# Optimization experiments

Hardware: AMD Instinct MI355X
Metric: run time of the kernel (lower is better)

The kernel has to match this reference:

```python
import jax, jax.numpy as jnp
import numpy as np

WS = 8         # window size (square)
SHIFT = 4      # shift size
NUM_HEADS = 8

def _layernorm(x, g, b, eps=1e-5):
    m = x.mean(-1, keepdims=True)
    v = ((x - m) ** 2).mean(-1, keepdims=True)
    return (x - m) / jnp.sqrt(v + eps) * g + b

def _rel_index():
    # relative_position_index for num_frames_q = num_frames_kv = 1 (d-term is 0)
    ch = np.arange(WS)
    coords = np.stack(np.meshgrid(ch, ch, indexing='ij'))      # (2, WS, WS)
    flat = coords.reshape(2, -1)                                 # (2, N)
    rel = flat[:, :, None] - flat[:, None, :]                    # (2, N, N)
    idx = (rel[0] + WS - 1) * (2 * WS - 1) + (rel[1] + WS - 1)   # (N, N)
    return jnp.asarray(idx, dtype=jnp.int32)

def setup_inputs() -> dict:
    key = jax.random.key(0)
    ks = jax.random.split(key, 16)
    B, D, H, W, C = 2, 2, 256, 256, 256
    hid = 4 * C
    nW = (H // WS) * (W // WS)
    N = WS * WS
    f = jax.random.normal
    return {
        'x': f(ks[0], (B, D, H, W, C), jnp.float32),
        'mask_matrix': f(ks[1], (nW, N, N), jnp.float32),
        'g1': jnp.ones((C,), jnp.float32),
        'b1': jnp.zeros((C,), jnp.float32),
        'qw': f(ks[2], (C, C), jnp.float32) * 0.02,
        'qb': jnp.zeros((C,), jnp.float32),
        'kvw': f(ks[3], (2 * C, C), jnp.float32) * 0.02,
        'kvb': jnp.zeros((2 * C,), jnp.float32),
        'pw': f(ks[4], (C, C), jnp.float32) * 0.02,
        'pb': jnp.zeros((C,), jnp.float32),
        'bias_table': f(ks[5], ((2 * WS - 1) ** 2, NUM_HEADS), jnp.float32) * 0.02,
        'g2': jnp.ones((C,), jnp.float32),
        'b2': jnp.zeros((C,), jnp.float32),
        'w1': f(ks[6], (hid, C), jnp.float32) * 0.02,
        'bi1': jnp.zeros((hid,), jnp.float32),
        'w2': f(ks[7], (C, hid), jnp.float32) * 0.02,
        'bi2': jnp.zeros((C,), jnp.float32),
    }

def reference(x, mask_matrix, g1, b1, qw, qb, kvw, kvb, pw, pb, bias_table, g2, b2, w1, bi1, w2, bi2):
    B, D, H, W, C = x.shape
    h = NUM_HEADS
    d = C // h
    N = WS * WS
    nH, nWc = H // WS, W // WS
    nwin = nH * nWc

    shortcut = x[:, 0]                       # (B, H, W, C)  (frame 0)
    xn = _layernorm(x, g1, b1)
    xs = jnp.roll(xn, (-SHIFT, -SHIFT), axis=(2, 3))   # cyclic shift

    # window partition: (B, D, H, W, C) -> (B*nwin, D, N, C)
    win = xs.reshape(B, D, nH, WS, nWc, WS, C)
    win = win.transpose(0, 2, 4, 1, 3, 5, 6).reshape(B * nwin, D, N, C)
    q_in = win[:, 0]                          # (B_, N, C) query = frame 0
    kv_in = win[:, 1]                         # (B_, N, C) kv    = frame 1

    q = (q_in @ qw.T + qb).reshape(-1, N, h, d).transpose(0, 2, 1, 3) * (d ** -0.5)
    kv = (kv_in @ kvw.T + kvb).reshape(-1, N, 2, h, d).transpose(2, 0, 3, 1, 4)
    k, v = kv[0], kv[1]                       # (B_, h, N, d)

    attn = jnp.einsum('bhnd,bhmd->bhnm', q, k)            # (B_, h, N, N)
    bias = bias_table[_rel_index()]                        # (N, N, h)
    attn = attn + bias.transpose(2, 0, 1)[None]
    attn = attn.reshape(B, nwin, h, N, N) + mask_matrix[None, :, None]
    attn = jax.nn.softmax(attn.reshape(-1, h, N, N), axis=-1)

    out = jnp.einsum('bhnm,bhmd->bhnd', attn, v)          # (B_, h, N, d)
    out = out.transpose(0, 2, 1, 3).reshape(-1, N, C)
    out = out @ pw.T + pb + q_in                           # residual inside attn

    # window reverse: (B*nwin, N, C) -> (B, H, W, C)
    out = out.reshape(B, nH, nWc, WS, WS, C).transpose(0, 1, 3, 2, 4, 5).reshape(B, H, W, C)
    out = jnp.roll(out, (SHIFT, SHIFT), axis=(1, 2))

    x1 = shortcut + out
    y = _layernorm(x1, g2, b2)
    y = jax.nn.gelu(y @ w1.T + bi1, approximate=False) @ w2.T + bi2
    return x1 + y
```

## Files before the change

kernel.cpp:

```cpp
#include <hip/hip_runtime.h>
#include <hip/hip_bf16.h>
#include <math.h>

#define SHIFT_ 4

typedef __attribute__((ext_vector_type(8))) short bh8;
typedef __attribute__((ext_vector_type(4))) short sh4;
typedef __attribute__((ext_vector_type(4))) float f4;
typedef __attribute__((ext_vector_type(8))) __bf16 bf8t;

static __device__ __forceinline__ f4 mfma16(bh8 a, bh8 b, f4 c){
  return __builtin_amdgcn_mfma_f32_16x16x32_bf16(
    __builtin_bit_cast(bf8t, a), __builtin_bit_cast(bf8t, b), c, 0, 0, 0);
}
static __device__ __forceinline__ unsigned short f2b(float f){
  unsigned u = __builtin_bit_cast(unsigned, f);
  u += 0x7fffu + ((u >> 16) & 1u);
  return (unsigned short)(u >> 16);
}
static __device__ __forceinline__ float b2f(unsigned short h){
  return __builtin_bit_cast(float, ((unsigned)h) << 16);
}
static __device__ __forceinline__ unsigned cvt_pk_bf16(float lo, float hi){
  unsigned r;
  asm("v_cvt_pk_bf16_f32 %0, %1, %2" : "=v"(r) : "v"(lo), "v"(hi));
  return r;
}
static __device__ __forceinline__ float gelu_f(float hv){
  float u = hv * (1.5957691216f + 0.0713548162f * hv * hv);
  return hv * __builtin_amdgcn_rcpf(1.f + __expf(-u));
}

__global__ __launch_bounds__(256) void prep_w(
    const float* __restrict__ qw, const float* __restrict__ kvw,
    const float* __restrict__ pw, const float* __restrict__ w1,
    const float* __restrict__ w2, unsigned short* __restrict__ wb){
  int i = blockIdx.x * 256 + threadIdx.x;
  float v;
  if      (i < 65536)  v = qw[i] * 0.17677669529663687f;
  else if (i < 196608) v = kvw[i - 65536];
  else if (i < 262144) v = pw[i - 196608];
  else if (i < 524288) v = w1[i - 262144];
  else                 v = w2[i - 524288];
  wb[i] = f2b(v);
}

__global__ __launch_bounds__(256) void ln1_win(
    const float* __restrict__ x, const float* __restrict__ g1,
    const float* __restrict__ b1,
    unsigned short* __restrict__ q_in, unsigned short* __restrict__ kv_in){
  int rid  = blockIdx.x * 4 + (threadIdx.x >> 6);
  int lane = threadIdx.x & 63;
  int d    = rid >> 17;
  int rem  = rid & 131071;
  int w = rem >> 6, n = rem & 63;
  int b = w >> 10, hb = (w >> 5) & 31, wbk = w & 31;
  int sh = (hb * 8 + (n >> 3) + SHIFT_) & 255;
  int sw = (wbk * 8 + (n & 7) + SHIFT_) & 255;
  const float* src = x + ((((size_t)(b * 2 + d)) * 256 + sh) * 256 + sw) * 256;
  float4 v = *(const float4*)(src + lane * 4);
  float s  = v.x + v.y + v.z + v.w;
  float ss = v.x * v.x + v.y * v.y + v.z * v.z + v.w * v.w;
  #pragma unroll
  for (int off = 1; off < 64; off <<= 1){ s += __shfl_xor(s, off); ss += __shfl_xor(ss, off); }
  float m    = s * (1.f / 256.f);
  float rstd = rsqrtf(ss * (1.f / 256.f) - m * m + 1e-5f);
  int c = lane * 4;
  float4 g  = *(const float4*)(g1 + c);
  float4 bb = *(const float4*)(b1 + c);
  sh4 o;
  o.x = (short)f2b((v.x - m) * rstd * g.x + bb.x);
  o.y = (short)f2b((v.y - m) * rstd * g.y + bb.y);
  o.z = (short)f2b((v.z - m) * rstd * g.z + bb.z);
  o.w = (short)f2b((v.w - m) * rstd * g.w + bb.w);
  unsigned short* dst = (d == 0 ? q_in : kv_in) + (size_t)rem * 256 + c;
  *(sh4*)dst = o;
}

template<int MODE, int NT>
__global__ __launch_bounds__(512, 4) void gemm_bt(
    const unsigned short* __restrict__ A, const unsigned short* __restrict__ Wt,
    const float* __restrict__ bias, float bias_scale,
    unsigned short* __restrict__ outb, unsigned short* __restrict__ vpl,
    float* __restrict__ outf, const unsigned short* __restrict__ qin,
    const float* __restrict__ xsrc){
  __shared__ unsigned short sA[128][64];
  __shared__ unsigned short sB[256][64];
  int m0 = blockIdx.x * 128;
  int tid = threadIdx.x, lane = tid & 63, wid = tid >> 6;
  int wm = wid >> 2, wn = wid & 3;
  int llo = lane & 15, lhi = lane >> 4;
  int lr = lane >> 3, lc = (lane & 7) * 8;
  const f4 FZ = {0.f, 0.f, 0.f, 0.f};
  for (int nt = 0; nt < NT; nt++){
    f4 acc[4][4];
    for (int i = 0; i < 4; i++) for (int j = 0; j < 4; j++) acc[i][j] = FZ;
    for (int t = 0; t < 4; t++){
      int k0 = t * 64;
      #pragma unroll
      for (int c = 0; c < 2; c++){
        int rr = wid * 16 + c * 8;
        __builtin_amdgcn_global_load_lds(
          (const __attribute__((address_space(1))) unsigned int*)(A + (size_t)(m0 + rr + lr) * 256 + k0 + lc),
          (__attribute__((address_space(3))) unsigned int*)&sA[rr][0], 16, 0, 0);
      }
      #pragma unroll
      for (int c = 0; c < 4; c++){
        int rb = wid * 32 + c * 8;
        __builtin_amdgcn_global_load_lds(
          (const __attribute__((address_space(1))) unsigned int*)(Wt + (size_t)(nt * 256 + rb + lr) * 256 + k0 + lc),
          (__attribute__((address_space(3))) unsigned int*)&sB[rb][0], 16, 0, 0);
      }
      __syncthreads();
      #pragma unroll
      for (int ks = 0; ks < 2; ks++){
        bh8 a[4], b[4];
        #pragma unroll
        for (int mi = 0; mi < 4; mi++) a[mi] = *(const bh8*)&sA[wm * 64 + mi * 16 + llo][ks * 32 + lhi * 8];
        #pragma unroll
        for (int nj = 0; nj < 4; nj++) b[nj] = *(const bh8*)&sB[wn * 64 + nj * 16 + llo][ks * 32 + lhi * 8];
        #pragma unroll
        for (int mi = 0; mi < 4; mi++)
          #pragma unroll
          for (int nj = 0; nj < 4; nj++){
            if (MODE < 2) acc[mi][nj] = mfma16(b[nj], a[mi], acc[mi][nj]);
            else          acc[mi][nj] = mfma16(a[mi], b[nj], acc[mi][nj]);
          }
      }
      __syncthreads();
    }
    if (MODE < 2){
      #pragma unroll
      for (int nj = 0; nj < 4; nj++){
        int cb = wn * 64 + nj * 16 + lhi * 4;
        int col = nt * 256 + cb;
        float4 bv = *(const float4*)(bias + col);
        #pragma unroll
        for (int mi = 0; mi < 4; mi++){
          int row = m0 + wm * 64 + mi * 16 + llo;
          float f0 = acc[mi][nj][0] + bv.x * bias_scale;
          float f1 = acc[mi][nj][1] + bv.y * bias_scale;
          float f2 = acc[mi][nj][2] + bv.z * bias_scale;
          float f3 = acc[mi][nj][3] + bv.w * bias_scale;
          uint2 p;
          p.x = cvt_pk_bf16(f0, f1);
          p.y = cvt_pk_bf16(f2, f3);
          if (MODE == 0 || nt == 0) *(uint2*)(outb + (size_t)row * 256 + cb) = p;
          else                      *(uint2*)(vpl  + (size_t)row * 256 + cb) = p;
        }
      }
    } else {
      #pragma unroll
      for (int mi = 0; mi < 4; mi++)
        #pragma unroll
        for (int nj = 0; nj < 4; nj++){
          int col = wn * 64 + nj * 16 + llo;
          float bv = bias[col] * bias_scale;
          #pragma unroll
          for (int r = 0; r < 4; r++){
            int row = m0 + wm * 64 + mi * 16 + lhi * 4 + r;
            int w = row >> 6, n = row & 63;
            int b = w >> 10, hb = (w >> 5) & 31, wbk = w & 31;
            int hh = (hb * 8 + (n >> 3) + SHIFT_) & 255;
            int ww = (wbk * 8 + (n & 7) + SHIFT_) & 255;
            float res = b2f(qin[(size_t)row * 256 + col]);
            float sc  = xsrc[((((size_t)(b * 2)) * 256 + hh) * 256 + ww) * 256 + col];
            outf[(((size_t)b * 256 + hh) * 256 + ww) * 256 + col] = acc[mi][nj][r] + bv + res + sc;
          }
        }
    }
  }
}

__global__ __launch_bounds__(256, 2) void attn_k(
    const unsigned short* __restrict__ q, const unsigned short* __restrict__ k,
    const unsigned short* __restrict__ v, const float* __restrict__ mask,
    const float* __restrict__ bias_table, unsigned short* __restrict__ aout){
  __shared__ unsigned short sMask[64][72];
  __shared__ unsigned short sVT[128][72];
  __shared__ unsigned short sP[4][64][72];
  __shared__ float sBias[4][225];
  int bid = blockIdx.x;
  int w = bid >> 1, hg = bid & 1;
  int tid = threadIdx.x, lane = tid & 63, wid = tid >> 6;
  int hd = hg * 4 + wid;
  int llo = lane & 15, lhi = lane >> 4;
  const unsigned short* qp = q + (size_t)w * 64 * 256 + hd * 32;
  const unsigned short* kp = k + (size_t)w * 64 * 256 + hd * 32;
  bh8 af[4], bf[4];
  #pragma unroll
  for (int mi = 0; mi < 4; mi++) af[mi] = *(const bh8*)(qp + (size_t)(mi * 16 + llo) * 256 + lhi * 8);
  #pragma unroll
  for (int nj = 0; nj < 4; nj++) bf[nj] = *(const bh8*)(kp + (size_t)(nj * 16 + llo) * 256 + lhi * 8);
  const float* mrow = mask + (size_t)(w & 1023) * 4096;
  #pragma unroll
  for (int i = 0; i < 2; i++){
    int base = (tid + i * 256) * 8;
    float4 u0 = *(const float4*)(mrow + base);
    float4 u1 = *(const float4*)(mrow + base + 4);
    int rr = base >> 6, cc = base & 63;
    uint4 p;
    p.x = cvt_pk_bf16(u0.x, u0.y); p.y = cvt_pk_bf16(u0.z, u0.w);
    p.z = cvt_pk_bf16(u1.x, u1.y); p.w = cvt_pk_bf16(u1.z, u1.w);
    *(uint4*)&sMask[rr][cc] = p;
  }
  {
    const unsigned short* vp = v + (size_t)w * 64 * 256 + hg * 128;
    #pragma unroll
    for (int it = 0; it < 4; it++){
      int idx = tid + it * 256;
      int n = idx >> 4, dc = (idx & 15) * 8;
      bh8 vv = *(const bh8*)(vp + (size_t)n * 256 + dc);
      #pragma unroll
      for (int j = 0; j < 8; j++) sVT[dc + j][n] = (unsigned short)vv[j];
    }
  }
  for (int i = lane; i < 225; i += 64) sBias[wid][i] = bias_table[i * 8 + hd];
  const f4 FZ = {0.f, 0.f, 0.f, 0.f};
  f4 acc[4][4];
  #pragma unroll
  for (int mi = 0; mi < 4; mi++)
    #pragma unroll
    for (int nj = 0; nj < 4; nj++)
      acc[mi][nj] = mfma16(af[mi], bf[nj], FZ);
  __syncthreads();
  #pragma unroll
  for (int mi = 0; mi < 4; mi++){
    #pragma unroll
    for (int r = 0; r < 4; r++){
      int rr = mi * 16 + lhi * 4 + r;
      int yi = rr >> 3, xi = rr & 7;
      float sv[4]; float mx = -1e30f;
      #pragma unroll
      for (int nj = 0; nj < 4; nj++){
        int cc = nj * 16 + llo;
        int idx = (yi - (cc >> 3) + 7) * 15 + (xi - (cc & 7) + 7);
        sv[nj] = acc[mi][nj][r] + sBias[wid][idx] + b2f(sMask[rr][cc]);
        mx = fmaxf(mx, sv[nj]);
      }
      #pragma unroll
      for (int off = 1; off < 16; off <<= 1) mx = fmaxf(mx, __shfl_xor(mx, off));
      float sum = 0.f;
      #pragma unroll
      for (int nj = 0; nj < 4; nj++){ sv[nj] = __expf(sv[nj] - mx); sum += sv[nj]; }
      #pragma unroll
      for (int off = 1; off < 16; off <<= 1) sum += __shfl_xor(sum, off);
      float inv = __builtin_amdgcn_rcpf(sum);
      #pragma unroll
      for (int nj = 0; nj < 4; nj++) sP[wid][rr][nj * 16 + llo] = f2b(sv[nj] * inv);
    }
  }
  f4 o[4][2];
  for (int mi = 0; mi < 4; mi++) for (int dj = 0; dj < 2; dj++) o[mi][dj] = FZ;
  #pragma unroll
  for (int ks = 0; ks < 2; ks++){
    bh8 pa[4], vb[2];
    #pragma unroll
    for (int mi = 0; mi < 4; mi++) pa[mi] = *(const bh8*)&sP[wid][mi * 16 + llo][ks * 32 + lhi * 8];
    #pragma unroll
    for (int dj = 0; dj < 2; dj++) vb[dj] = *(const bh8*)&sVT[wid * 32 + dj * 16 + llo][ks * 32 + lhi * 8];
    #pragma unroll
    for (int mi = 0; mi < 4; mi++)
      #pragma unroll
      for (int dj = 0; dj < 2; dj++)
        o[mi][dj] = mfma16(pa[mi], vb[dj], o[mi][dj]);
  }
  #pragma unroll
  for (int mi = 0; mi < 4; mi++)
    for (int dj = 0; dj < 2; dj++)
      for (int r = 0; r < 4; r++){
        int rr = mi * 16 + lhi * 4 + r, dd = dj * 16 + llo;
        aout[((size_t)w * 64 + rr) * 256 + hd * 32 + dd] = f2b(o[mi][dj][r]);
      }
}

__global__ __launch_bounds__(256) void ln2_k(
    const float* __restrict__ x1, const float* __restrict__ g2,
    const float* __restrict__ b2, unsigned short* __restrict__ xn){
  int rid  = blockIdx.x * 4 + (threadIdx.x >> 6);
  int lane = threadIdx.x & 63;
  const float* xr = x1 + (size_t)rid * 256;
  float4 v = *(const float4*)(xr + lane * 4);
  float s  = v.x + v.y + v.z + v.w;
  float ss = v.x * v.x + v.y * v.y + v.z * v.z + v.w * v.w;
  #pragma unroll
  for (int off = 1; off < 64; off <<= 1){ s += __shfl_xor(s, off); ss += __shfl_xor(ss, off); }
  float m    = s * (1.f / 256.f);
  float rstd = rsqrtf(ss * (1.f / 256.f) - m * m + 1e-5f);
  int c = lane * 4;
  float4 g  = *(const float4*)(g2 + c);
  float4 bb = *(const float4*)(b2 + c);
  sh4 o;
  o.x = (short)f2b((v.x - m) * rstd * g.x + bb.x);
  o.y = (short)f2b((v.y - m) * rstd * g.y + bb.y);
  o.z = (short)f2b((v.z - m) * rstd * g.z + bb.z);
  o.w = (short)f2b((v.w - m) * rstd * g.w + bb.w);
  *(sh4*)(xn + (size_t)rid * 256 + c) = o;
}

template<int KSTEPS, int EPI, int BIASF>
__global__ __launch_bounds__(256, 3) void mlp_gemm(
    const unsigned short* __restrict__ A, int lda,
    const unsigned short* __restrict__ Bw, int ldb,
    const float* __restrict__ bias,
    unsigned short* __restrict__ outb, int ldo,
    float* __restrict__ outf){
  __shared__ unsigned short sA[128][64];
  __shared__ unsigned short sB[128][64];
  int n0 = blockIdx.x * 128, m0 = blockIdx.y * 128;
  int tid = threadIdx.x, lane = tid & 63, wid = tid >> 6;
  int wm = wid >> 1, wn = wid & 1;
  int llo = lane & 15, lhi = lane >> 4;
  int lr = lane >> 3, lc = (lane & 7) * 8;
  const f4 FZ = {0.f, 0.f, 0.f, 0.f};
  f4 acc[4][4];
  for (int i = 0; i < 4; i++) for (int j = 0; j < 4; j++) acc[i][j] = FZ;

  for (int t = 0; t < KSTEPS; t++){
    int k0 = t * 64;
    #pragma unroll
    for (int c = 0; c < 4; c++){
      int rr = wid * 32 + c * 8 + lr;
      __builtin_amdgcn_global_load_lds(
        (const __attribute__((address_space(1))) unsigned int*)(A + (size_t)(m0 + rr) * lda + k0 + lc),
        (__attribute__((address_space(3))) unsigned int*)&sA[wid * 32 + c * 8][0], 16, 0, 0);
      __builtin_amdgcn_global_load_lds(
        (const __attribute__((address_space(1))) unsigned int*)(Bw + (size_t)(n0 + rr) * ldb + k0 + lc),
        (__attribute__((address_space(3))) unsigned int*)&sB[wid * 32 + c * 8][0], 16, 0, 0);
    }
    __syncthreads();
    #pragma unroll
    for (int ks = 0; ks < 2; ks++){
      bh8 a[4], b[4];
      #pragma unroll
      for (int mi = 0; mi < 4; mi++) a[mi] = *(const bh8*)&sA[wm * 64 + mi * 16 + llo][ks * 32 + lhi * 8];
      #pragma unroll
      for (int nj = 0; nj < 4; nj++) b[nj] = *(const bh8*)&sB[wn * 64 + nj * 16 + llo][ks * 32 + lhi * 8];
      #pragma unroll
      for (int mi = 0; mi < 4; mi++)
        #pragma unroll
        for (int nj = 0; nj < 4; nj++){
          if (EPI == 0) acc[mi][nj] = mfma16(b[nj], a[mi], acc[mi][nj]);
          else          acc[mi][nj] = mfma16(a[mi], b[nj], acc[mi][nj]);
        }
    }
    __syncthreads();
  }
  if (EPI == 0){
    #pragma unroll
    for (int nj = 0; nj < 4; nj++){
      int cb = n0 + wn * 64 + nj * 16 + lhi * 4;
      float4 bv = *(const float4*)(bias + cb);
      #pragma unroll
      for (int mi = 0; mi < 4; mi++){
        int row = m0 + wm * 64 + mi * 16 + llo;
        float g0 = gelu_f(acc[mi][nj][0] + bv.x);
        float g1 = gelu_f(acc[mi][nj][1] + bv.y);
        float g2 = gelu_f(acc[mi][nj][2] + bv.z);
        float g3 = gelu_f(acc[mi][nj][3] + bv.w);
        uint2 p;
        p.x = cvt_pk_bf16(g0, g1);
        p.y = cvt_pk_bf16(g2, g3);
        *(uint2*)(outb + (size_t)row * ldo + cb) = p;
      }
    }
  } else {
    #pragma unroll
    for (int mi = 0; mi < 4; mi++)
      #pragma unroll
      for (int nj = 0; nj < 4; nj++){
        int col = n0 + wn * 64 + nj * 16 + llo;
        float bv = BIASF ? bias[col] : 0.f;
        #pragma unroll
        for (int r = 0; r < 4; r++){
          int row = m0 + wm * 64 + mi * 16 + lhi * 4 + r;
          outf[(size_t)row * 256 + col] += acc[mi][nj][r] + bv;
        }
      }
  }
}

extern "C" void kernel_launch(void* const* d_in, const int* in_sizes, int n_in,
                              void* d_out, int out_size, void* d_ws, size_t ws_size,
                              hipStream_t stream){
  const float* x          = (const float*)d_in[0];
  const float* mask       = (const float*)d_in[1];
  const float* g1         = (const float*)d_in[2];
  const float* b1         = (const float*)d_in[3];
  const float* qw         = (const float*)d_in[4];
  const float* qb         = (const float*)d_in[5];
  const float* kvw        = (const float*)d_in[6];
  const float* kvb        = (const float*)d_in[7];
  const float* pw         = (const float*)d_in[8];
  const float* pb         = (const float*)d_in[9];
  const float* bias_table = (const float*)d_in[10];
  const float* g2         = (const float*)d_in[11];
  const float* b2         = (const float*)d_in[12];
  const float* w1         = (const float*)d_in[13];
  const float* bi1        = (const float*)d_in[14];
  const float* w2         = (const float*)d_in[15];
  const float* bi2        = (const float*)d_in[16];
  float* out = (float*)d_out;
  char* ws = (char*)d_ws;
  const long long MB = 1048576LL;
  unsigned short* wb    = (unsigned short*)(ws);
  unsigned short* q_in  = (unsigned short*)(ws + (long long)(1.5 * MB));
  unsigned short* kv_in = (unsigned short*)(ws + (long long)(65.5 * MB));
  unsigned short* qbuf  = (unsigned short*)(ws + (long long)(129.5 * MB));
  unsigned short* kbuf  = (unsigned short*)(ws + (long long)(193.5 * MB));
  unsigned short* vbuf  = (unsigned short*)(ws + (long long)(257.5 * MB));
  unsigned short* aoutb = kv_in;
  unsigned short* xn    = vbuf;
  unsigned short* Hh    = q_in;

  prep_w<<<3072, 256, 0, stream>>>(qw, kvw, pw, w1, w2, wb);
  ln1_win<<<65536, 256, 0, stream>>>(x, g1, b1, q_in, kv_in);
  gemm_bt<0, 1><<<1024, 512, 0, stream>>>(q_in, wb, qb, 0.17677669529663687f,
                                          qbuf, nullptr, nullptr, nullptr, nullptr);
  gemm_bt<1, 2><<<1024, 512, 0, stream>>>(kv_in, wb + 65536, kvb, 1.0f,
                                          kbuf, vbuf, nullptr, nullptr, nullptr);
  attn_k<<<4096, 256, 0, stream>>>(qbuf, kbuf, vbuf, mask, bias_table, aoutb);
  gemm_bt<2, 1><<<1024, 512, 0, stream>>>(aoutb, wb + 196608, pb, 1.0f,
                                          nullptr, nullptr, out, q_in, x);
  ln2_k<<<32768, 256, 0, stream>>>(out, g2, b2, xn);
  const unsigned short* w1b = wb + 262144;
  const unsigned short* w2b = wb + 524288;
  for (int h = 0; h < 2; h++){
    const long long R = (long long)h * 65536;
    mlp_gemm<4, 0, 0><<<dim3(8, 512), 256, 0, stream>>>(xn + R * 256, 256, w1b, 256,
                                                        bi1, Hh, 1024, nullptr);
    mlp_gemm<16, 1, 1><<<dim3(2, 512), 256, 0, stream>>>(Hh, 1024, w2b, 1024,
                                                         bi2, nullptr, 0, out + R * 256);
  }
}
```

Measured before the change: 768.9 us.

## Double-buffer LDS tiles in GEMM kernels and shrink MLP chunk size

Both the attention projection GEMMs and the MLP GEMMs now double-buffer their shared-memory tiles, prefetching the next K-slice with async global-to-LDS loads while the MFMA work runs on the current slice. This removes one barrier per step and hides load latency. gemm_bt moves from 512-thread blocks with a 128x256 tile to 256-thread blocks that loop over 128-wide N tiles. The MLP is split into four row chunks instead of two, so the hidden buffer fits in cache better. The costs are lower occupancy from doubled LDS and a lower launch_bounds, plus more kernel launches.

```diff
diff --git a/kernel.cpp b/kernel.cpp
--- a/kernel.cpp
+++ b/kernel.cpp
@@ -29,6 +29,11 @@
 static __device__ __forceinline__ float gelu_f(float hv){
   float u = hv * (1.5957691216f + 0.0713548162f * hv * hv);
   return hv * __builtin_amdgcn_rcpf(1.f + __expf(-u));
+}
+static __device__ __forceinline__ void glds16(const unsigned short* g, unsigned short* l){
+  __builtin_amdgcn_global_load_lds(
+    (const __attribute__((address_space(1))) unsigned int*)g,
+    (__attribute__((address_space(3))) unsigned int*)l, 16, 0, 0);
 }
 
 __global__ __launch_bounds__(256) void prep_w(
@@ -78,97 +83,101 @@
 }
 
 template<int MODE, int NT>
-__global__ __launch_bounds__(512, 4) void gemm_bt(
+__global__ __launch_bounds__(256, 2) void gemm_bt(
     const unsigned short* __restrict__ A, const unsigned short* __restrict__ Wt,
     const float* __restrict__ bias, float bias_scale,
     unsigned short* __restrict__ outb, unsigned short* __restrict__ vpl,
     float* __restrict__ outf, const unsigned short* __restrict__ qin,
     const float* __restrict__ xsrc){
-  __shared__ unsigned short sA[128][64];
-  __shared__ unsigned short sB[256][64];
+  __shared__ unsigned short sA[2][128][64];
+  __shared__ unsigned short sB[2][128][64];
   int m0 = blockIdx.x * 128;
   int tid = threadIdx.x, lane = tid & 63, wid = tid >> 6;
-  int wm = wid >> 2, wn = wid & 3;
+  int wm = wid >> 1, wn = wid & 1;
   int llo = lane & 15, lhi = lane >> 4;
   int lr = lane >> 3, lc = (lane & 7) * 8;
+  const int TT = NT * 4;
+  #pragma unroll
+  for (int c = 0; c < 4; c++){
+    int rr = wid * 32 + c * 8;
+    glds16(A  + (size_t)(m0 + rr + lr) * 256 + lc, &sA[0][rr][0]);
+    glds16(Wt + (size_t)(rr + lr) * 256 + lc,      &sB[0][rr][0]);
+  }
+  __syncthreads();
   const f4 FZ = {0.f, 0.f, 0.f, 0.f};
-  for (int nt = 0; nt < NT; nt++){
-    f4 acc[4][4];
-    for (int i = 0; i < 4; i++) for (int j = 0; j < 4; j++) acc[i][j] = FZ;
-    for (int t = 0; t < 4; t++){
-      int k0 = t * 64;
-      #pragma unroll
-      for (int c = 0; c < 2; c++){
-        int rr = wid * 16 + c * 8;
-        __builtin_amdgcn_global_load_lds(
-          (const __attribute__((address_space(1))) unsigned int*)(A + (size_t)(m0 + rr + lr) * 256 + k0 + lc),
-          (__attribute__((address_space(3))) unsigned int*)&sA[rr][0], 16, 0, 0);
-      }
+  f4 acc[4][4];
+  for (int i = 0; i < 4; i++) for (int j = 0; j < 4; j++) acc[i][j] = FZ;
+  for (int tt = 0; tt < TT; ++tt){
+    int cur = tt & 1;
+    if (tt + 1 < TT){
+      int t1 = (tt + 1) & 3, n1 = (tt + 1) >> 2;
       #pragma unroll
       for (int c = 0; c < 4; c++){
-        int rb = wid * 32 + c * 8;
-        __builtin_amdgcn_global_load_lds(
-          (const __attribute__((address_space(1))) unsigned int*)(Wt + (size_t)(nt * 256 + rb + lr) * 256 + k0 + lc),
-          (__attribute__((address_space(3))) unsigned int*)&sB[rb][0], 16, 0, 0);
-      }
-      __syncthreads();
-      #pragma unroll
-      for (int ks = 0; ks < 2; ks++){
-        bh8 a[4], b[4];
+        int rr = wid * 32 + c * 8;
+        glds16(A  + (size_t)(m0 + rr + lr) * 256 + t1 * 64 + lc,       &sA[cur ^ 1][rr][0]);
+        glds16(Wt + (size_t)(n1 * 128 + rr + lr) * 256 + t1 * 64 + lc, &sB[cur ^ 1][rr][0]);
+      }
+    }
+    #pragma unroll
+    for (int ks = 0; ks < 2; ks++){
+      bh8 a[4], b[4];
+      #pragma unroll
+      for (int mi = 0; mi < 4; mi++) a[mi] = *(const bh8*)&sA[cur][wm * 64 + mi * 16 + llo][ks * 32 + lhi * 8];
+      #pragma unroll
+      for (int nj = 0; nj < 4; nj++) b[nj] = *(const bh8*)&sB[cur][wn * 64 + nj * 16 + llo][ks * 32 + lhi * 8];
+      #pragma unroll
+      for (int mi = 0; mi < 4; mi++)
         #pragma unroll
-        for (int mi = 0; mi < 4; mi++) a[mi] = *(const bh8*)&sA[wm * 64 + mi * 16 + llo][ks * 32 + lhi * 8];
+        for (int nj = 0; nj < 4; nj++){
+          if (MODE < 2) acc[mi][nj] = mfma16(b[nj], a[mi], acc[mi][nj]);
+          else          acc[mi][nj] = mfma16(a[mi], b[nj], acc[mi][nj]);
+        }
+    }
+    if ((tt & 3) == 3){
+      int nt = tt >> 2;
+      if (MODE < 2){
         #pragma unroll
-        for (int nj = 0; nj < 4; nj++) b[nj] = *(const bh8*)&sB[wn * 64 + nj * 16 + llo][ks * 32 + lhi * 8];
+        for (int nj = 0; nj < 4; nj++){
+          int cb = wn * 64 + nj * 16 + lhi * 4;
+          int col = nt * 128 + cb;
+          float4 bv = *(const float4*)(bias + col);
+          #pragma unroll
+          for (int mi = 0; mi < 4; mi++){
+            int row = m0 + wm * 64 + mi * 16 + llo;
+            float f0 = acc[mi][nj][0] + bv.x * bias_scale;
+            float f1 = acc[mi][nj][1] + bv.y * bias_scale;
+            float f2 = acc[mi][nj][2] + bv.z * bias_scale;
+            float f3 = acc[mi][nj][3] + bv.w * bias_scale;
+            uint2 p;
+            p.x = cvt_pk_bf16(f0, f1);
+            p.y = cvt_pk_bf16(f2, f3);
+            if (MODE == 0 || col < 256) *(uint2*)(outb + (size_t)row * 256 + col) = p;
+            else                        *(uint2*)(vpl  + (size_t)row * 256 + (col - 256)) = p;
+          }
+        }
+      } else {
         #pragma unroll
         for (int mi = 0; mi < 4; mi++)
           #pragma unroll
           for (int nj = 0; nj < 4; nj++){
-            if (MODE < 2) acc[mi][nj] = mfma16(b[nj], a[mi], acc[mi][nj]);
-            else          acc[mi][nj] = mfma16(a[mi], b[nj], acc[mi][nj]);
+            int col = nt * 128 + wn * 64 + nj * 16 + llo;
+            float bv = bias[col] * bias_scale;
+            #pragma unroll
+            for (int r = 0; r < 4; r++){
+              int row = m0 + wm * 64 + mi * 16 + lhi * 4 + r;
+              int w = row >> 6, n = row & 63;
+              int b = w >> 10, hb = (w >> 5) & 31, wbk = w & 31;
+              int hh = (hb * 8 + (n >> 3) + SHIFT_) & 255;
+              int ww = (wbk * 8 + (n & 7) + SHIFT_) & 255;
+              float res = b2f(qin[(size_t)row * 256 + col]);
+              float sc  = xsrc[((((size_t)(b * 2)) * 256 + hh) * 256 + ww) * 256 + col];
+              outf[(((size_t)b * 256 + hh) * 256 + ww) * 256 + col] = acc[mi][nj][r] + bv + res + sc;
+            }
           }
       }
-      __syncthreads();
-    }
-    if (MODE < 2){
-      #pragma unroll
-      for (int nj = 0; nj < 4; nj++){
-        int cb = wn * 64 + nj * 16 + lhi * 4;
-        int col = nt * 256 + cb;
-        float4 bv = *(const float4*)(bias + col);
-        #pragma unroll
-        for (int mi = 0; mi < 4; mi++){
-          int row = m0 + wm * 64 + mi * 16 + llo;
-          float f0 = acc[mi][nj][0] + bv.x * bias_scale;
-          float f1 = acc[mi][nj][1] + bv.y * bias_scale;
-          float f2 = acc[mi][nj][2] + bv.z * bias_scale;
-          float f3 = acc[mi][nj][3] + bv.w * bias_scale;
-          uint2 p;
-          p.x = cvt_pk_bf16(f0, f1);
-          p.y = cvt_pk_bf16(f2, f3);
-          if (MODE == 0 || nt == 0) *(uint2*)(outb + (size_t)row * 256 + cb) = p;
-          else                      *(uint2*)(vpl  + (size_t)row * 256 + cb) = p;
-        }
-      }
-    } else {
-      #pragma unroll
-      for (int mi = 0; mi < 4; mi++)
-        #pragma unroll
-        for (int nj = 0; nj < 4; nj++){
-          int col = wn * 64 + nj * 16 + llo;
-          float bv = bias[col] * bias_scale;
-          #pragma unroll
-          for (int r = 0; r < 4; r++){
-            int row = m0 + wm * 64 + mi * 16 + lhi * 4 + r;
-            int w = row >> 6, n = row & 63;
-            int b = w >> 10, hb = (w >> 5) & 31, wbk = w & 31;
-            int hh = (hb * 8 + (n >> 3) + SHIFT_) & 255;
-            int ww = (wbk * 8 + (n & 7) + SHIFT_) & 255;
-            float res = b2f(qin[(size_t)row * 256 + col]);
-            float sc  = xsrc[((((size_t)(b * 2)) * 256 + hh) * 256 + ww) * 256 + col];
-            outf[(((size_t)b * 256 + hh) * 256 + ww) * 256 + col] = acc[mi][nj][r] + bv + res + sc;
-          }
-        }
-    }
+      for (int i = 0; i < 4; i++) for (int j = 0; j < 4; j++) acc[i][j] = FZ;
+    }
+    __syncthreads();
   }
 }
 
@@ -299,43 +308,48 @@
 }
 
 template<int KSTEPS, int EPI, int BIASF>
-__global__ __launch_bounds__(256, 3) void mlp_gemm(
+__global__ __launch_bounds__(256, 2) void mlp_gemm(
     const unsigned short* __restrict__ A, int lda,
     const unsigned short* __restrict__ Bw, int ldb,
     const float* __restrict__ bias,
     unsigned short* __restrict__ outb, int ldo,
     float* __restrict__ outf){
-  __shared__ unsigned short sA[128][64];
-  __shared__ unsigned short sB[128][64];
+  __shared__ unsigned short sA[2][128][64];
+  __shared__ unsigned short sB[2][128][64];
   int n0 = blockIdx.x * 128, m0 = blockIdx.y * 128;
   int tid = threadIdx.x, lane = tid & 63, wid = tid >> 6;
   int wm = wid >> 1, wn = wid & 1;
   int llo = lane & 15, lhi = lane >> 4;
   int lr = lane >> 3, lc = (lane & 7) * 8;
+  #pragma unroll
+  for (int c = 0; c < 4; c++){
+    int rr = wid * 32 + c * 8;
+    glds16(A  + (size_t)(m0 + rr + lr) * lda + lc, &sA[0][rr][0]);
+    glds16(Bw + (size_t)(n0 + rr + lr) * ldb + lc, &sB[0][rr][0]);
+  }
+  __syncthreads();
   const f4 FZ = {0.f, 0.f, 0.f, 0.f};
   f4 acc[4][4];
   for (int i = 0; i < 4; i++) for (int j = 0; j < 4; j++) acc[i][j] = FZ;
 
   for (int t = 0; t < KSTEPS; t++){
-    int k0 = t * 64;
-    #pragma unroll
-    for (int c = 0; c < 4; c++){
-      int rr = wid * 32 + c * 8 + lr;
-      __builtin_amdgcn_global_load_lds(
-        (const __attribute__((address_space(1))) unsigned int*)(A + (size_t)(m0 + rr) * lda + k0 + lc),
-        (__attribute__((address_space(3))) unsigned int*)&sA[wid * 32 + c * 8][0], 16, 0, 0);
-      __builtin_amdgcn_global_load_lds(
-        (const __attribute__((address_space(1))) unsigned int*)(Bw + (size_t)(n0 + rr) * ldb + k0 + lc),
-        (__attribute__((address_space(3))) unsigned int*)&sB[wid * 32 + c * 8][0], 16, 0, 0);
-    }
-    __syncthreads();
+    int cur = t & 1;
+    if (t + 1 < KSTEPS){
+      int k1 = (t + 1) * 64;
+      #pragma unroll
+      for (int c = 0; c < 4; c++){
+        int rr = wid * 32 + c * 8;
+        glds16(A  + (size_t)(m0 + rr + lr) * lda + k1 + lc, &sA[cur ^ 1][rr][0]);
+        glds16(Bw + (size_t)(n0 + rr + lr) * ldb + k1 + lc, &sB[cur ^ 1][rr][0]);
+      }
+    }
     #pragma unroll
     for (int ks = 0; ks < 2; ks++){
       bh8 a[4], b[4];
       #pragma unroll
-      for (int mi = 0; mi < 4; mi++) a[mi] = *(const bh8*)&sA[wm * 64 + mi * 16 + llo][ks * 32 + lhi * 8];
-      #pragma unroll
-      for (int nj = 0; nj < 4; nj++) b[nj] = *(const bh8*)&sB[wn * 64 + nj * 16 + llo][ks * 32 + lhi * 8];
+      for (int mi = 0; mi < 4; mi++) a[mi] = *(const bh8*)&sA[cur][wm * 64 + mi * 16 + llo][ks * 32 + lhi * 8];
+      #pragma unroll
+      for (int nj = 0; nj < 4; nj++) b[nj] = *(const bh8*)&sB[cur][wn * 64 + nj * 16 + llo][ks * 32 + lhi * 8];
       #pragma unroll
       for (int mi = 0; mi < 4; mi++)
         #pragma unroll
@@ -415,21 +429,21 @@
 
   prep_w<<<3072, 256, 0, stream>>>(qw, kvw, pw, w1, w2, wb);
   ln1_win<<<65536, 256, 0, stream>>>(x, g1, b1, q_in, kv_in);
-  gemm_bt<0, 1><<<1024, 512, 0, stream>>>(q_in, wb, qb, 0.17677669529663687f,
+  gemm_bt<0, 2><<<1024, 256, 0, stream>>>(q_in, wb, qb, 0.17677669529663687f,
                                           qbuf, nullptr, nullptr, nullptr, nullptr);
-  gemm_bt<1, 2><<<1024, 512, 0, stream>>>(kv_in, wb + 65536, kvb, 1.0f,
+  gemm_bt<1, 4><<<1024, 256, 0, stream>>>(kv_in, wb + 65536, kvb, 1.0f,
                                           kbuf, vbuf, nullptr, nullptr, nullptr);
   attn_k<<<4096, 256, 0, stream>>>(qbuf, kbuf, vbuf, mask, bias_table, aoutb);
-  gemm_bt<2, 1><<<1024, 512, 0, stream>>>(aoutb, wb + 196608, pb, 1.0f,
+  gemm_bt<2, 2><<<1024, 256, 0, stream>>>(aoutb, wb + 196608, pb, 1.0f,
                                           nullptr, nullptr, out, q_in, x);
   ln2_k<<<32768, 256, 0, stream>>>(out, g2, b2, xn);
   const unsigned short* w1b = wb + 262144;
   const unsigned short* w2b = wb + 524288;
-  for (int h = 0; h < 2; h++){
-    const long long R = (long long)h * 65536;
-    mlp_gemm<4, 0, 0><<<dim3(8, 512), 256, 0, stream>>>(xn + R * 256, 256, w1b, 256,
+  for (int h = 0; h < 4; h++){
+    const long long R = (long long)h * 32768;
+    mlp_gemm<4, 0, 0><<<dim3(8, 256), 256, 0, stream>>>(xn + R * 256, 256, w1b, 256,
                                                         bi1, Hh, 1024, nullptr);
-    mlp_gemm<16, 1, 1><<<dim3(2, 512), 256, 0, stream>>>(Hh, 1024, w2b, 1024,
+    mlp_gemm<16, 1, 1><<<dim3(2, 256), 256, 0, stream>>>(Hh, 1024, w2b, 1024,
                                                          bi2, nullptr, 0, out + R * 256);
   }
 }
```

Result: slower. 834.3 us (+8.5%).

## Fuse Q and KV projections into one kernel and LayerNorm2 into proj GEMM

Applied to the files above, without the earlier changes.

Merges the separate Q and KV projection GEMM launches into a single kernel that loops over the three output slices. It also folds the second LayerNorm into the output-projection GEMM epilogue, computing row statistics through shuffles and LDS and writing both the fp32 residual and the bf16 normalized activations. This removes one launch and the full re-read of the fp32 x1 tensor by the standalone ln2 kernel. In exchange the epilogue does extra LDS reductions and syncs, and it still writes with scattered per-lane stores.

```diff
diff --git a/kernel.cpp b/kernel.cpp
--- a/kernel.cpp
+++ b/kernel.cpp
@@ -29,6 +29,11 @@
 static __device__ __forceinline__ float gelu_f(float hv){
   float u = hv * (1.5957691216f + 0.0713548162f * hv * hv);
   return hv * __builtin_amdgcn_rcpf(1.f + __expf(-u));
+}
+static __device__ __forceinline__ void glds16(const unsigned short* g, unsigned short* l){
+  __builtin_amdgcn_global_load_lds(
+    (const __attribute__((address_space(1))) unsigned int*)g,
+    (__attribute__((address_space(3))) unsigned int*)l, 16, 0, 0);
 }
 
 __global__ __launch_bounds__(256) void prep_w(
@@ -77,13 +82,12 @@
   *(sh4*)dst = o;
 }
 
-template<int MODE, int NT>
-__global__ __launch_bounds__(512, 4) void gemm_bt(
-    const unsigned short* __restrict__ A, const unsigned short* __restrict__ Wt,
-    const float* __restrict__ bias, float bias_scale,
-    unsigned short* __restrict__ outb, unsigned short* __restrict__ vpl,
-    float* __restrict__ outf, const unsigned short* __restrict__ qin,
-    const float* __restrict__ xsrc){
+__global__ __launch_bounds__(512, 4) void qkv_gemm(
+    const unsigned short* __restrict__ q_in, const unsigned short* __restrict__ kv_in,
+    const unsigned short* __restrict__ wpack,
+    const float* __restrict__ qbias, const float* __restrict__ kvbias,
+    unsigned short* __restrict__ qo, unsigned short* __restrict__ ko,
+    unsigned short* __restrict__ vo){
   __shared__ unsigned short sA[128][64];
   __shared__ unsigned short sB[256][64];
   int m0 = blockIdx.x * 128;
@@ -92,7 +96,12 @@
   int llo = lane & 15, lhi = lane >> 4;
   int lr = lane >> 3, lc = (lane & 7) * 8;
   const f4 FZ = {0.f, 0.f, 0.f, 0.f};
-  for (int nt = 0; nt < NT; nt++){
+  for (int nt = 0; nt < 3; nt++){
+    const unsigned short* A  = (nt == 0) ? q_in : kv_in;
+    const unsigned short* Wt = wpack + nt * 65536;
+    const float* bias = (nt == 0) ? qbias : kvbias + (nt - 1) * 256;
+    unsigned short* outb = (nt == 0) ? qo : (nt == 1 ? ko : vo);
+    float bscale = (nt == 0) ? 0.17677669529663687f : 1.f;
     f4 acc[4][4];
     for (int i = 0; i < 4; i++) for (int j = 0; j < 4; j++) acc[i][j] = FZ;
     for (int t = 0; t < 4; t++){
@@ -100,16 +109,12 @@
       #pragma unroll
       for (int c = 0; c < 2; c++){
         int rr = wid * 16 + c * 8;
-        __builtin_amdgcn_global_load_lds(
-          (const __attribute__((address_space(1))) unsigned int*)(A + (size_t)(m0 + rr + lr) * 256 + k0 + lc),
-          (__attribute__((address_space(3))) unsigned int*)&sA[rr][0], 16, 0, 0);
+        glds16(A + (size_t)(m0 + rr + lr) * 256 + k0 + lc, &sA[rr][0]);
       }
       #pragma unroll
       for (int c = 0; c < 4; c++){
         int rb = wid * 32 + c * 8;
-        __builtin_amdgcn_global_load_lds(
-          (const __attribute__((address_space(1))) unsigned int*)(Wt + (size_t)(nt * 256 + rb + lr) * 256 + k0 + lc),
-          (__attribute__((address_space(3))) unsigned int*)&sB[rb][0], 16, 0, 0);
+        glds16(Wt + (size_t)(rb + lr) * 256 + k0 + lc, &sB[rb][0]);
       }
       __syncthreads();
       #pragma unroll
@@ -122,52 +127,27 @@
         #pragma unroll
         for (int mi = 0; mi < 4; mi++)
           #pragma unroll
-          for (int nj = 0; nj < 4; nj++){
-            if (MODE < 2) acc[mi][nj] = mfma16(b[nj], a[mi], acc[mi][nj]);
-            else          acc[mi][nj] = mfma16(a[mi], b[nj], acc[mi][nj]);
-          }
+          for (int nj = 0; nj < 4; nj++)
+            acc[mi][nj] = mfma16(b[nj], a[mi], acc[mi][nj]);
       }
       __syncthreads();
     }
-    if (MODE < 2){
-      #pragma unroll
-      for (int nj = 0; nj < 4; nj++){
-        int cb = wn * 64 + nj * 16 + lhi * 4;
-        int col = nt * 256 + cb;
-        float4 bv = *(const float4*)(bias + col);
-        #pragma unroll
-        for (int mi = 0; mi < 4; mi++){
-          int row = m0 + wm * 64 + mi * 16 + llo;
-          float f0 = acc[mi][nj][0] + bv.x * bias_scale;
-          float f1 = acc[mi][nj][1] + bv.y * bias_scale;
-          float f2 = acc[mi][nj][2] + bv.z * bias_scale;
-          float f3 = acc[mi][nj][3] + bv.w * bias_scale;
-          uint2 p;
-          p.x = cvt_pk_bf16(f0, f1);
-          p.y = cvt_pk_bf16(f2, f3);
-          if (MODE == 0 || nt == 0) *(uint2*)(outb + (size_t)row * 256 + cb) = p;
-          else                      *(uint2*)(vpl  + (size_t)row * 256 + cb) = p;
-        }
-      }
-    } else {
-      #pragma unroll
-      for (int mi = 0; mi < 4; mi++)
-        #pragma unroll
-        for (int nj = 0; nj < 4; nj++){
-          int col = wn * 64 + nj * 16 + llo;
-          float bv = bias[col] * bias_scale;
-          #pragma unroll
-          for (int r = 0; r < 4; r++){
-            int row = m0 + wm * 64 + mi * 16 + lhi * 4 + r;
-            int w = row >> 6, n = row & 63;
-            int b = w >> 10, hb = (w >> 5) & 31, wbk = w & 31;
-            int hh = (hb * 8 + (n >> 3) + SHIFT_) & 255;
-            int ww = (wbk * 8 + (n & 7) + SHIFT_) & 255;
-            float res = b2f(qin[(size_t)row * 256 + col]);
-            float sc  = xsrc[((((size_t)(b * 2)) * 256 + hh) * 256 + ww) * 256 + col];
-            outf[(((size_t)b * 256 + hh) * 256 + ww) * 256 + col] = acc[mi][nj][r] + bv + res + sc;
-          }
-        }
+    #pragma unroll
+    for (int nj = 0; nj < 4; nj++){
+      int cb = wn * 64 + nj * 16 + lhi * 4;
+      float4 bv = *(const float4*)(bias + cb);
+      #pragma unroll
+      for (int mi = 0; mi < 4; mi++){
+        int row = m0 + wm * 64 + mi * 16 + llo;
+        float f0 = acc[mi][nj][0] + bv.x * bscale;
+        float f1 = acc[mi][nj][1] + bv.y * bscale;
+        float f2 = acc[mi][nj][2] + bv.z * bscale;
+        float f3 = acc[mi][nj][3] + bv.w * bscale;
+        uint2 p;
+        p.x = cvt_pk_bf16(f0, f1);
+        p.y = cvt_pk_bf16(f2, f3);
+        *(uint2*)(outb + (size_t)row * 256 + cb) = p;
+      }
     }
   }
 }
@@ -274,28 +254,123 @@
       }
 }
 
-__global__ __launch_bounds__(256) void ln2_k(
-    const float* __restrict__ x1, const float* __restrict__ g2,
-    const float* __restrict__ b2, unsigned short* __restrict__ xn){
-  int rid  = blockIdx.x * 4 + (threadIdx.x >> 6);
-  int lane = threadIdx.x & 63;
-  const float* xr = x1 + (size_t)rid * 256;
-  float4 v = *(const float4*)(xr + lane * 4);
-  float s  = v.x + v.y + v.z + v.w;
-  float ss = v.x * v.x + v.y * v.y + v.z * v.z + v.w * v.w;
-  #pragma unroll
-  for (int off = 1; off < 64; off <<= 1){ s += __shfl_xor(s, off); ss += __shfl_xor(ss, off); }
-  float m    = s * (1.f / 256.f);
-  float rstd = rsqrtf(ss * (1.f / 256.f) - m * m + 1e-5f);
-  int c = lane * 4;
-  float4 g  = *(const float4*)(g2 + c);
-  float4 bb = *(const float4*)(b2 + c);
-  sh4 o;
-  o.x = (short)f2b((v.x - m) * rstd * g.x + bb.x);
-  o.y = (short)f2b((v.y - m) * rstd * g.y + bb.y);
-  o.z = (short)f2b((v.z - m) * rstd * g.z + bb.z);
-  o.w = (short)f2b((v.w - m) * rstd * g.w + bb.w);
-  *(sh4*)(xn + (size_t)rid * 256 + c) = o;
+__global__ __launch_bounds__(512, 4) void pgemm_ln(
+    const unsigned short* __restrict__ A, const unsigned short* __restrict__ Wt,
+    const float* __restrict__ bias,
+    float* __restrict__ outf, const unsigned short* __restrict__ qin,
+    const float* __restrict__ xsrc,
+    const float* __restrict__ g2, const float* __restrict__ b2,
+    unsigned short* __restrict__ xn){
+  __shared__ unsigned short sA[128][64];
+  __shared__ unsigned short sB[256][64];
+  __shared__ float sSum[128][4];
+  __shared__ float sSq[128][4];
+  __shared__ float sMV[128][2];
+  int m0 = blockIdx.x * 128;
+  int tid = threadIdx.x, lane = tid & 63, wid = tid >> 6;
+  int wm = wid >> 2, wn = wid & 3;
+  int llo = lane & 15, lhi = lane >> 4;
+  int lr = lane >> 3, lc = (lane & 7) * 8;
+  const f4 FZ = {0.f, 0.f, 0.f, 0.f};
+  f4 acc[4][4];
+  for (int i = 0; i < 4; i++) for (int j = 0; j < 4; j++) acc[i][j] = FZ;
+  for (int t = 0; t < 4; t++){
+    int k0 = t * 64;
+    #pragma unroll
+    for (int c = 0; c < 2; c++){
+      int rr = wid * 16 + c * 8;
+      glds16(A + (size_t)(m0 + rr + lr) * 256 + k0 + lc, &sA[rr][0]);
+    }
+    #pragma unroll
+    for (int c = 0; c < 4; c++){
+      int rb = wid * 32 + c * 8;
+      glds16(Wt + (size_t)(rb + lr) * 256 + k0 + lc, &sB[rb][0]);
+    }
+    __syncthreads();
+    #pragma unroll
+    for (int ks = 0; ks < 2; ks++){
+      bh8 a[4], b[4];
+      #pragma unroll
+      for (int mi = 0; mi < 4; mi++) a[mi] = *(const bh8*)&sA[wm * 64 + mi * 16 + llo][ks * 32 + lhi * 8];
+      #pragma unroll
+      for (int nj = 0; nj < 4; nj++) b[nj] = *(const bh8*)&sB[wn * 64 + nj * 16 + llo][ks * 32 + lhi * 8];
+      #pragma unroll
+      for (int mi = 0; mi < 4; mi++)
+        #pragma unroll
+        for (int nj = 0; nj < 4; nj++)
+          acc[mi][nj] = mfma16(a[mi], b[nj], acc[mi][nj]);
+    }
+    __syncthreads();
+  }
+  #pragma unroll
+  for (int mi = 0; mi < 4; mi++){
+    #pragma unroll
+    for (int r = 0; r < 4; r++){
+      int row = m0 + wm * 64 + mi * 16 + lhi * 4 + r;
+      int w = row >> 6, n = row & 63;
+      int b = w >> 10, hb = (w >> 5) & 31, wbk = w & 31;
+      int hh = (hb * 8 + (n >> 3) + SHIFT_) & 255;
+      int ww = (wbk * 8 + (n & 7) + SHIFT_) & 255;
+      const float* sc = xsrc + (((size_t)(b * 2) * 256 + hh) * 256 + ww) * 256;
+      #pragma unroll
+      for (int nj = 0; nj < 4; nj++){
+        int col = wn * 64 + nj * 16 + llo;
+        acc[mi][nj][r] += bias[col] + b2f(qin[(size_t)row * 256 + col]) + sc[col];
+      }
+    }
+  }
+  #pragma unroll
+  for (int mi = 0; mi < 4; mi++){
+    #pragma unroll
+    for (int r = 0; r < 4; r++){
+      float s = 0.f, sq = 0.f;
+      #pragma unroll
+      for (int nj = 0; nj < 4; nj++){ float v = acc[mi][nj][r]; s += v; sq += v * v; }
+      #pragma unroll
+      for (int off = 1; off < 16; off <<= 1){ s += __shfl_xor(s, off); sq += __shfl_xor(sq, off); }
+      if (llo == 0){
+        int rl = wm * 64 + mi * 16 + lhi * 4 + r;
+        sSum[rl][wn] = s; sSq[rl][wn] = sq;
+      }
+    }
+  }
+  __syncthreads();
+  if (tid < 128){
+    float s = sSum[tid][0] + sSum[tid][1] + sSum[tid][2] + sSum[tid][3];
+    float q = sSq[tid][0] + sSq[tid][1] + sSq[tid][2] + sSq[tid][3];
+    float mean = s * (1.f / 256.f);
+    float var  = q * (1.f / 256.f) - mean * mean;
+    sMV[tid][0] = mean;
+    sMV[tid][1] = rsqrtf(var + 1e-5f);
+  }
+  __syncthreads();
+  float g2v[4], b2v[4];
+  #pragma unroll
+  for (int nj = 0; nj < 4; nj++){
+    int col = wn * 64 + nj * 16 + llo;
+    g2v[nj] = g2[col]; b2v[nj] = b2[col];
+  }
+  #pragma unroll
+  for (int mi = 0; mi < 4; mi++){
+    #pragma unroll
+    for (int r = 0; r < 4; r++){
+      int rl = wm * 64 + mi * 16 + lhi * 4 + r;
+      int row = m0 + rl;
+      float mean = sMV[rl][0], rstd = sMV[rl][1];
+      int w = row >> 6, n = row & 63;
+      int b = w >> 10, hb = (w >> 5) & 31, wbk = w & 31;
+      int hh = (hb * 8 + (n >> 3) + SHIFT_) & 255;
+      int ww = (wbk * 8 + (n & 7) + SHIFT_) & 255;
+      size_t rbase = (((size_t)b * 256 + hh) * 256 + ww) * 256;
+      #pragma unroll
+      for (int nj = 0; nj < 4; nj++){
+        int col = wn * 64 + nj * 16 + llo;
+        float v = acc[mi][nj][r];
+        outf[rbase + col] = v;
+        xn[rbase + col] = f2b((v - mean) * rstd * g2v[nj] + b2v[nj]);
+      }
+    }
+  }
 }
 
 template<int KSTEPS, int EPI, int BIASF>
@@ -321,12 +396,8 @@
     #pragma unroll
     for (int c = 0; c < 4; c++){
       int rr = wid * 32 + c * 8 + lr;
-      __builtin_amdgcn_global_load_lds(
-        (const __attribute__((address_space(1))) unsigned int*)(A + (size_t)(m0 + rr) * lda + k0 + lc),
-        (__attribute__((address_space(3))) unsigned int*)&sA[wid * 32 + c * 8][0], 16, 0, 0);
-      __builtin_amdgcn_global_load_lds(
-        (const __attribute__((address_space(1))) unsigned int*)(Bw + (size_t)(n0 + rr) * ldb + k0 + lc),
-        (__attribute__((address_space(3))) unsigned int*)&sB[wid * 32 + c * 8][0], 16, 0, 0);
+      glds16(A  + (size_t)(m0 + rr) * lda + k0 + lc, &sA[wid * 32 + c * 8][0]);
+      glds16(Bw + (size_t)(n0 + rr) * ldb + k0 + lc, &sB[wid * 32 + c * 8][0]);
     }
     __syncthreads();
     #pragma unroll
@@ -415,14 +486,10 @@
 
   prep_w<<<3072, 256, 0, stream>>>(qw, kvw, pw, w1, w2, wb);
   ln1_win<<<65536, 256, 0, stream>>>(x, g1, b1, q_in, kv_in);
-  gemm_bt<0, 1><<<1024, 512, 0, stream>>>(q_in, wb, qb, 0.17677669529663687f,
-                                          qbuf, nullptr, nullptr, nullptr, nullptr);
-  gemm_bt<1, 2><<<1024, 512, 0, stream>>>(kv_in, wb + 65536, kvb, 1.0f,
-                                          kbuf, vbuf, nullptr, nullptr, nullptr);
+  qkv_gemm<<<1024, 512, 0, stream>>>(q_in, kv_in, wb, qb, kvb, qbuf, kbuf, vbuf);
   attn_k<<<4096, 256, 0, stream>>>(qbuf, kbuf, vbuf, mask, bias_table, aoutb);
-  gemm_bt<2, 1><<<1024, 512, 0, stream>>>(aoutb, wb + 196608, pb, 1.0f,
-                                          nullptr, nullptr, out, q_in, x);
-  ln2_k<<<32768, 256, 0, stream>>>(out, g2, b2, xn);
+  pgemm_ln<<<1024, 512, 0, stream>>>(aoutb, wb + 196608, pb, out, q_in, x,
+                                     g2, b2, xn);
   const unsigned short* w1b = wb + 262144;
   const unsigned short* w2b = wb + 524288;
   for (int h = 0; h < 2; h++){
```

After: 876.6 us. 1.14x slower.
